# Kernel tuning notes

Hardware: AMD Instinct MI355X
Metric: run time of the kernel (lower is better)

Reference implementation:

```python
import jax, jax.numpy as jnp
import numpy as np

N_HEADS = 16


def setup_inputs() -> dict:
    key = jax.random.key(0)
    k0, k1, k2 = jax.random.split(key, 3)
    B, S, D = 8, 1024, 1024
    x = jax.random.normal(k0, (B, S, D), dtype=jnp.float32)
    W_qkv = jax.random.normal(k1, (D, 3 * D), dtype=jnp.float32) * 0.02
    b_qkv = jnp.zeros((3 * D,), dtype=jnp.float32)
    W_proj = jax.random.normal(k2, (D, D), dtype=jnp.float32) * 0.02
    b_proj = jnp.zeros((D,), dtype=jnp.float32)
    return {"x": x, "W_qkv": W_qkv, "b_qkv": b_qkv, "W_proj": W_proj, "b_proj": b_proj}


def reference(x, W_qkv, b_qkv, W_proj, b_proj):
    B, S, D = x.shape
    H = N_HEADS
    hd = D // H
    scale = hd ** (-0.5)
    # qkv projection: (B,S,3D) -> (3,B,H,S,hd)
    qkv = x @ W_qkv + b_qkv
    qkv = qkv.reshape(B, S, 3, H, hd).transpose(2, 0, 3, 1, 4)
    q, k, v = qkv[0], qkv[1], qkv[2]
    # explicit materialized attention scores (B,H,S,S), softmax over keys
    scores = jnp.einsum("bhqd,bhkd->bhqk", q, k) * scale
    attn = jax.nn.softmax(scores, axis=-1)
    # weighted values -> concat heads -> output projection
    out = jnp.einsum("bhqk,bhkd->bhqd", attn, v)
    out = out.transpose(0, 2, 1, 3).reshape(B, S, D)
    return out @ W_proj + b_proj
```

## Files before the change

kernel.cpp:

```cpp
#include <hip/hip_runtime.h>
#include <hip/hip_bf16.h>

typedef __bf16 bf16_t;
typedef __attribute__((ext_vector_type(8))) __bf16 bf16x8;
typedef __attribute__((ext_vector_type(4))) float f32x4;
typedef __attribute__((ext_vector_type(16))) float f32x16;

#define QSCALE 0.18033688011112042f
#define RESCALE_THR 11.5f

#define OFF_XB      ((size_t)0)
#define OFF_WQKVT   ((size_t)16777216)
#define OFF_WPROJT  ((size_t)(16777216 + 6291456))
#define OFF_Q       ((size_t)(16777216 + 6291456 + 2097152))
#define OFF_K       (OFF_Q + (size_t)16777216)
#define OFF_V       (OFF_K + (size_t)16777216)
#define OFF_O       OFF_XB

typedef const __attribute__((address_space(1))) void* as1cv;
typedef __attribute__((address_space(3))) void* as3v;

__device__ __forceinline__ void load_lds16(const void* g, void* l) {
  __builtin_amdgcn_global_load_lds((as1cv)g, (as3v)l, 16, 0, 0);
}

__device__ __forceinline__ f32x4 mfma16(bf16x8 a, bf16x8 b, f32x4 c) {
  return __builtin_amdgcn_mfma_f32_16x16x32_bf16(a, b, c, 0, 0, 0);
}
__device__ __forceinline__ f32x16 mfma32(bf16x8 a, bf16x8 b, f32x16 c) {
  return __builtin_amdgcn_mfma_f32_32x32x16_bf16(a, b, c, 0, 0, 0);
}

__device__ __forceinline__ float fexp2(float x) { return __builtin_amdgcn_exp2f(x); }

__device__ __forceinline__ unsigned pack2bf(float a, float b) {
  union { bf16_t h[2]; unsigned u; } x;
  x.h[0] = (bf16_t)a; x.h[1] = (bf16_t)b;
  return x.u;
}

__device__ __forceinline__ bf16x8 frag_from_words(unsigned w0, unsigned w1,
                                                  unsigned w2, unsigned w3) {
  union { unsigned u[4]; bf16x8 v; } x;
  x.u[0] = w0; x.u[1] = w1; x.u[2] = w2; x.u[3] = w3;
  return x.v;
}

__device__ __forceinline__ bf16x8 ldsr(const bf16_t* lds, int row, int slotbyte) {
  return *(const bf16x8*)((const char*)lds + row * 128 +
                          (slotbyte ^ ((row & 7) << 4)));
}


__global__ __launch_bounds__(256) void cvt_bf16_kernel(
    const float* __restrict__ in, bf16_t* __restrict__ out, int n8) {
  int i = blockIdx.x * blockDim.x + threadIdx.x;
  if (i >= n8) return;
  const float4* p = (const float4*)in + (size_t)i * 2;
  float4 a = p[0], b = p[1];
  bf16x8 o;
  o[0] = (bf16_t)a.x; o[1] = (bf16_t)a.y; o[2] = (bf16_t)a.z; o[3] = (bf16_t)a.w;
  o[4] = (bf16_t)b.x; o[5] = (bf16_t)b.y; o[6] = (bf16_t)b.z; o[7] = (bf16_t)b.w;
  ((bf16x8*)out)[i] = o;
}

__global__ __launch_bounds__(256) void transpose_cvt2(
    const float* __restrict__ W1, bf16_t* __restrict__ Wt1,
    const float* __restrict__ W2, bf16_t* __restrict__ Wt2) {
  __shared__ float t[32][33];
  const int bx = blockIdx.x;
  const float* W;  bf16_t* Wt;  int cols, c0;
  if (bx < 96) { W = W1; Wt = Wt1; cols = 3072; c0 = bx * 32; }
  else         { W = W2; Wt = Wt2; cols = 1024; c0 = (bx - 96) * 32; }
  const int r0 = blockIdx.y * 32;
  const int tx = threadIdx.x, ty = threadIdx.y;
  for (int rr = ty; rr < 32; rr += 8)
    t[rr][tx] = W[(size_t)(r0 + rr) * cols + c0 + tx];
  __syncthreads();
  for (int rr = ty; rr < 32; rr += 8)
    Wt[(size_t)(c0 + rr) * 1024 + r0 + tx] = (bf16_t)t[tx][rr];
}


__device__ __forceinline__ void gemm_mainloop_1024(
    const bf16_t* __restrict__ A, const bf16_t* __restrict__ Bt,
    int m0, int n0, bf16_t* Alds, bf16_t* Blds, f32x4 acc[4][4]) {
  const int tid = threadIdx.x;
  const int w = tid >> 6, lane = tid & 63;
  const int wr = w >> 1, wc = w & 1;
  const int lr = lane & 15, lg = lane >> 4;
#pragma unroll
  for (int m = 0; m < 4; ++m)
#pragma unroll
    for (int n = 0; n < 4; ++n)
      acc[m][n] = f32x4{0.f, 0.f, 0.f, 0.f};

  const int crow = lane >> 3;
  const int cels = (((lane & 7) ^ crow) * 8);
  const int rx = (lr & 7) << 4;

  for (int kt = 0; kt < 16; ++kt) {
    const int k0 = kt * 64;
#pragma unroll
    for (int it = 0; it < 4; ++it) {
      const int c = it * 4 + w;
      const int rA = c * 8 + crow;
      load_lds16(A + (size_t)(m0 + rA) * 1024 + k0 + cels, (char*)Alds + c * 1024);
      load_lds16(Bt + (size_t)(n0 + rA) * 1024 + k0 + cels, (char*)Blds + c * 1024);
    }
    asm volatile("s_waitcnt vmcnt(0)" ::: "memory");
    __syncthreads();

    bf16x8 af[4][2], bfr[4][2];
#pragma unroll
    for (int m = 0; m < 4; ++m)
#pragma unroll
      for (int kk = 0; kk < 2; ++kk)
        af[m][kk] = *(const bf16x8*)((const char*)Alds + (wr * 64 + m * 16 + lr) * 128 +
                                     ((kk * 64 + lg * 16) ^ rx));
#pragma unroll
    for (int n = 0; n < 4; ++n)
#pragma unroll
      for (int kk = 0; kk < 2; ++kk)
        bfr[n][kk] = *(const bf16x8*)((const char*)Blds + (wc * 64 + n * 16 + lr) * 128 +
                                      ((kk * 64 + lg * 16) ^ rx));
#pragma unroll
    for (int kk = 0; kk < 2; ++kk)
#pragma unroll
      for (int m = 0; m < 4; ++m)
#pragma unroll
        for (int n = 0; n < 4; ++n)
          acc[m][n] = mfma16(af[m][kk], bfr[n][kk], acc[m][n]);
    __syncthreads();
  }
}

__device__ __forceinline__ void xcd_remap(int bid, int MT_PER, int* mt, int* nt) {
  const int r = bid & 7, q = bid >> 3;
  *mt = r * MT_PER + (q & (MT_PER - 1));
  *nt = q / MT_PER;
}


__global__ __launch_bounds__(256) void gemm_qkv(
    const bf16_t* __restrict__ A, const bf16_t* __restrict__ Bt,
    const float* __restrict__ bias,
    bf16_t* __restrict__ Qh, bf16_t* __restrict__ Kh, bf16_t* __restrict__ Vt) {
  __shared__ alignas(128) bf16_t Alds[128 * 64];
  __shared__ alignas(128) bf16_t Blds[128 * 64];
  int mt, nt;
  xcd_remap(blockIdx.x, 8, &mt, &nt);
  const int m0 = mt * 128, n0 = nt * 128;
  f32x4 acc[4][4];
  gemm_mainloop_1024(A, Bt, m0, n0, Alds, Blds, acc);

  const int tid = threadIdx.x, w = tid >> 6, lane = tid & 63;
  const int wr = w >> 1, wc = w & 1, lr = lane & 15, lg = lane >> 4;
  const int section = n0 >> 10;
#pragma unroll
  for (int n = 0; n < 4; ++n) {
    const int c = n0 + wc * 64 + n * 16 + lr;
    const float bi = bias[c];
    const int d1024 = c & 1023;
    const int h = d1024 >> 6, d = d1024 & 63;
#pragma unroll
    for (int m = 0; m < 4; ++m) {
#pragma unroll
      for (int j = 0; j < 4; ++j) {
        const int r = m0 + wr * 64 + m * 16 + lg * 4 + j;
        const int b = r >> 10, s = r & 1023;
        const size_t hb = ((size_t)(b * 16 + h)) << 16;
        const float v = acc[m][n][j] + bi;
        if (section == 0)      Qh[hb + (size_t)s * 64 + d] = (bf16_t)(v * QSCALE);
        else if (section == 1) Kh[hb + (size_t)s * 64 + d] = (bf16_t)v;
        else                   Vt[hb + (size_t)d * 1024 + s] = (bf16_t)v;
      }
    }
  }
}


__global__ __launch_bounds__(256) void gemm_out(
    const bf16_t* __restrict__ A, const bf16_t* __restrict__ Bt,
    const float* __restrict__ bias, float* __restrict__ out) {
  __shared__ alignas(128) bf16_t Alds[128 * 64];
  __shared__ alignas(128) bf16_t Blds[128 * 64];
  int mt, nt;
  xcd_remap(blockIdx.x, 8, &mt, &nt);
  const int m0 = mt * 128, n0 = nt * 128;
  f32x4 acc[4][4];
  gemm_mainloop_1024(A, Bt, m0, n0, Alds, Blds, acc);

  const int tid = threadIdx.x, w = tid >> 6, lane = tid & 63;
  const int wr = w >> 1, wc = w & 1, lr = lane & 15, lg = lane >> 4;
#pragma unroll
  for (int n = 0; n < 4; ++n) {
    const int c = n0 + wc * 64 + n * 16 + lr;
    const float bi = bias[c];
#pragma unroll
    for (int m = 0; m < 4; ++m)
#pragma unroll
      for (int j = 0; j < 4; ++j) {
        const int r = m0 + wr * 64 + m * 16 + lg * 4 + j;
        out[(size_t)r * 1024 + c] = acc[m][n][j] + bi;
      }
  }
}


__global__ __launch_bounds__(256, 4) void attn_kernel(
    const bf16_t* __restrict__ Qh, const bf16_t* __restrict__ Kh,
    const bf16_t* __restrict__ Vt, bf16_t* __restrict__ Ob) {
  __shared__ alignas(128) bf16_t Klds[2][64 * 64];
  __shared__ alignas(128) bf16_t Vlds[2][64 * 64];

  const int x = blockIdx.x;
  const int bh = ((x & 7) << 4) | (x >> 6);
  const int qt = (x >> 3) & 7;
  const int b = bh >> 4, h = bh & 15;
  const int tid = threadIdx.x, w = tid >> 6, lane = tid & 63;
  const int q31 = lane & 31, hi = lane >> 5;
  const size_t base = (size_t)bh << 16;

  const int qrow0 = qt * 128 + w * 32;

  bf16x8 qf[4];
#pragma unroll
  for (int c = 0; c < 4; ++c)
    qf[c] = *(const bf16x8*)(Qh + base + (size_t)(qrow0 + q31) * 64 + hi * 8 + 16 * c);

  f32x16 oacc0, oacc1;
#pragma unroll
  for (int r = 0; r < 16; ++r) { oacc0[r] = 0.f; oacc1[r] = 0.f; }
  float mreg = -1e30f, lreg = 0.f;

  const int srow = lane >> 3;
  const int sslot = (((lane & 7) ^ srow) << 3);

#define STAGE_KV(bsel, kt_)                                                        \
  do {                                                                             \
    _Pragma("unroll")                                                              \
    for (int it = 0; it < 2; ++it) {                                               \
      const int c = it * 4 + w;                                                    \
      const int r = c * 8 + srow;                                                  \
      load_lds16(Kh + base + (size_t)((kt_) * 64 + r) * 64 + sslot,                \
                 (char*)&Klds[bsel][0] + c * 1024);                                \
      load_lds16(Vt + base + (size_t)r * 1024 + (kt_) * 64 + sslot,                \
                 (char*)&Vlds[bsel][0] + c * 1024);                                \
    }                                                                              \
  } while (0)

  STAGE_KV(0, 0);
  asm volatile("s_waitcnt vmcnt(0)" ::: "memory");
  __syncthreads();
  int cur = 0;

  for (int kt = 0; kt < 16; ++kt) {
    if (kt + 1 < 16) STAGE_KV(cur ^ 1, kt + 1);

    const bf16_t* Kb = &Klds[cur][0];
    const bf16_t* Vb = &Vlds[cur][0];

    f32x16 st0, st1;
#pragma unroll
    for (int r = 0; r < 16; ++r) { st0[r] = 0.f; st1[r] = 0.f; }
#pragma unroll
    for (int c = 0; c < 4; ++c) {
      const int sb = hi * 16 + 32 * c;
      bf16x8 k0 = ldsr(Kb, q31, sb);
      bf16x8 k1 = ldsr(Kb, 32 + q31, sb);
      __builtin_amdgcn_s_setprio(1);
      st0 = mfma32(k0, qf[c], st0);
      st1 = mfma32(k1, qf[c], st1);
      __builtin_amdgcn_s_setprio(0);
    }

    float mx[8];
#pragma unroll
    for (int r = 0; r < 8; ++r)
      mx[r] = fmaxf(fmaxf(st0[r], st0[r + 8]), fmaxf(st1[r], st1[r + 8]));
#pragma unroll
    for (int r = 0; r < 4; ++r) mx[r] = fmaxf(mx[r], mx[r + 4]);
    float tm = fmaxf(fmaxf(mx[0], mx[1]), fmaxf(mx[2], mx[3]));
    tm = fmaxf(tm, __shfl_xor(tm, 32));

    if (!__all(tm - mreg <= RESCALE_THR)) {
      const float mnew = fmaxf(mreg, tm);
      const float corr = fexp2(mreg - mnew);
      lreg *= corr;
#pragma unroll
      for (int r = 0; r < 16; ++r) { oacc0[r] *= corr; oacc1[r] *= corr; }
      mreg = mnew;
    }

    bf16x8 pa[4];
    float psum = 0.f;
#define GROUP(KC, STV, BASE)                                                   \
    {                                                                          \
      const float e0 = fexp2(STV[BASE + 0] - mreg);                            \
      const float e1 = fexp2(STV[BASE + 1] - mreg);                            \
      const float e2 = fexp2(STV[BASE + 2] - mreg);                            \
      const float e3 = fexp2(STV[BASE + 3] - mreg);                            \
      const float e4 = fexp2(STV[BASE + 4] - mreg);                            \
      const float e5 = fexp2(STV[BASE + 5] - mreg);                            \
      const float e6 = fexp2(STV[BASE + 6] - mreg);                            \
      const float e7 = fexp2(STV[BASE + 7] - mreg);                            \
      psum += ((e0 + e1) + (e2 + e3)) + ((e4 + e5) + (e6 + e7));               \
      unsigned wa = pack2bf(e0, e1), wb = pack2bf(e4, e5);                     \
      asm volatile("v_permlane32_swap_b32 %0, %1" : "+v"(wa), "+v"(wb));       \
      unsigned wc = pack2bf(e2, e3), wd = pack2bf(e6, e7);                     \
      asm volatile("v_permlane32_swap_b32 %0, %1" : "+v"(wc), "+v"(wd));       \
      pa[KC] = frag_from_words(wa, wc, wb, wd);                                \
    }
    GROUP(0, st0, 0)
    GROUP(1, st0, 8)
    GROUP(2, st1, 0)
    GROUP(3, st1, 8)
#undef GROUP
    lreg += psum + __shfl_xor(psum, 32);

#pragma unroll
    for (int kc = 0; kc < 4; ++kc) {
      const int sb = hi * 16 + 32 * kc;
      bf16x8 v0 = ldsr(Vb, q31, sb);
      bf16x8 v1 = ldsr(Vb, 32 + q31, sb);
      __builtin_amdgcn_s_setprio(1);
      oacc0 = mfma32(v0, pa[kc], oacc0);
      oacc1 = mfma32(v1, pa[kc], oacc1);
      __builtin_amdgcn_s_setprio(0);
    }

    asm volatile("s_waitcnt vmcnt(0)" ::: "memory");
    __syncthreads();
    cur ^= 1;
  }
#undef STAGE_KV

  const float inv = 1.0f / lreg;
  const int s_tok = qrow0 + q31;
  bf16_t* obase = Ob + (size_t)(b * 1024 + s_tok) * 1024 + h * 64;
#pragma unroll
  for (int i = 0; i < 8; ++i) {
    const int dbase = ((2 * i) & 3) + 8 * ((2 * i) >> 2) + 4 * hi;
    *(unsigned*)(obase + dbase) =
        pack2bf(oacc0[2 * i] * inv, oacc0[2 * i + 1] * inv);
    *(unsigned*)(obase + 32 + dbase) =
        pack2bf(oacc1[2 * i] * inv, oacc1[2 * i + 1] * inv);
  }
}


extern "C" void kernel_launch(void* const* d_in, const int* in_sizes, int n_in,
                              void* d_out, int out_size, void* d_ws, size_t ws_size,
                              hipStream_t stream) {
  const float* x     = (const float*)d_in[0];
  const float* Wqkv  = (const float*)d_in[1];
  const float* bqkv  = (const float*)d_in[2];
  const float* Wproj = (const float*)d_in[3];
  const float* bproj = (const float*)d_in[4];
  float* out = (float*)d_out;
  char* ws = (char*)d_ws;

  bf16_t* Xb  = (bf16_t*)(ws + OFF_XB);
  bf16_t* Wqt = (bf16_t*)(ws + OFF_WQKVT);
  bf16_t* Wpt = (bf16_t*)(ws + OFF_WPROJT);
  bf16_t* Qh  = (bf16_t*)(ws + OFF_Q);
  bf16_t* Kh  = (bf16_t*)(ws + OFF_K);
  bf16_t* Vt  = (bf16_t*)(ws + OFF_V);
  bf16_t* Ob  = (bf16_t*)(ws + OFF_O);

  cvt_bf16_kernel<<<4096, 256, 0, stream>>>(x, Xb, 1048576);
  transpose_cvt2<<<dim3(128, 32), dim3(32, 8), 0, stream>>>(Wqkv, Wqt, Wproj, Wpt);
  gemm_qkv<<<1536, 256, 0, stream>>>(Xb, Wqt, bqkv, Qh, Kh, Vt);
  attn_kernel<<<1024, 256, 0, stream>>>(Qh, Kh, Vt, Ob);
  gemm_out<<<512, 256, 0, stream>>>(Ob, Wpt, bproj, out);
}
```

Measured before the change: 176.7 us.

## Overlap next K-tile global-to-LDS loads with MFMA compute in GEMM mainloop

Restructures the GEMM mainloop so all LDS fragments are read into registers first, followed by a barrier. The next K-tile's global_load_lds is then issued before the MFMA block, so memory traffic overlaps with matrix math while a single LDS buffer is kept. The MFMA section also runs at raised wave priority via s_setprio. This relies on explicit waitcnt and barrier ordering to avoid LDS races, and it raises register pressure because the fragments stay live across the loads.

```diff
diff --git a/kernel.cpp b/kernel.cpp
--- a/kernel.cpp
+++ b/kernel.cpp
@@ -99,17 +99,24 @@
   const int cels = (((lane & 7) ^ crow) * 8);
   const int rx = (lr & 7) << 4;
 
+#define STAGE_AB(kt_)                                                            \
+  do {                                                                           \
+    _Pragma("unroll")                                                            \
+    for (int it = 0; it < 4; ++it) {                                             \
+      const int c = it * 4 + w;                   \
+      const int rA = c * 8 + crow;                          \
+      load_lds16(A + (size_t)(m0 + rA) * 1024 + (kt_) * 64 + cels,               \
+                 (char*)Alds + c * 1024);                                        \
+      load_lds16(Bt + (size_t)(n0 + rA) * 1024 + (kt_) * 64 + cels,              \
+                 (char*)Blds + c * 1024);                                        \
+    }                                                                            \
+  } while (0)
+
+  STAGE_AB(0);
+
   for (int kt = 0; kt < 16; ++kt) {
-    const int k0 = kt * 64;
-#pragma unroll
-    for (int it = 0; it < 4; ++it) {
-      const int c = it * 4 + w;
-      const int rA = c * 8 + crow;
-      load_lds16(A + (size_t)(m0 + rA) * 1024 + k0 + cels, (char*)Alds + c * 1024);
-      load_lds16(Bt + (size_t)(n0 + rA) * 1024 + k0 + cels, (char*)Blds + c * 1024);
-    }
     asm volatile("s_waitcnt vmcnt(0)" ::: "memory");
-    __syncthreads();
+    asm volatile("s_barrier" ::: "memory");
 
     bf16x8 af[4][2], bfr[4][2];
 #pragma unroll
@@ -124,6 +131,13 @@
       for (int kk = 0; kk < 2; ++kk)
         bfr[n][kk] = *(const bf16x8*)((const char*)Blds + (wc * 64 + n * 16 + lr) * 128 +
                                       ((kk * 64 + lg * 16) ^ rx));
+    asm volatile("s_waitcnt lgkmcnt(0)" ::: "memory");
+    __builtin_amdgcn_sched_barrier(0);
+    asm volatile("s_barrier" ::: "memory");
+
+    if (kt + 1 < 16) STAGE_AB(kt + 1);
+
+    __builtin_amdgcn_s_setprio(1);
 #pragma unroll
     for (int kk = 0; kk < 2; ++kk)
 #pragma unroll
@@ -131,8 +145,10 @@
 #pragma unroll
         for (int n = 0; n < 4; ++n)
           acc[m][n] = mfma16(af[m][kk], bfr[n][kk], acc[m][n]);
-    __syncthreads();
-  }
+    __builtin_amdgcn_s_setprio(0);
+    __builtin_amdgcn_sched_barrier(0);
+  }
+#undef STAGE_AB
 }
 
 __device__ __forceinline__ void xcd_remap(int bid, int MT_PER, int* mt, int* nt) {
```

New measurement: 171.1 us. -3.2%, faster.
